# Optimization experiments

Measured on AMD Instinct MI355X. Metric: run time of the kernel, lower is better.

Reference implementation:

```python
import jax, jax.numpy as jnp
import numpy as np

N_NODES = 50000
N_EDGES = 800000
N_S = 32          # 0e channels in node feats
N_V = 16          # 1o channels in node feats
NB = 8            # radial bessel basis size
H = 64            # MLP hidden
S_OUT = N_S + N_V           # 48 scalar message channels (filtered 0e + dot path)
V_OUT = N_V + N_S + N_V     # 64 vector message channels (filtered 1o + sxY1 + vxY2)
NUM_IRREPS = S_OUT + V_OUT  # 112, gated by radial MLP
AVG_NEIGH = 16.0


def setup_inputs() -> dict:
    key = jax.random.key(0)
    ks = jax.random.split(key, 8)
    # scale so edge lengths fall mostly inside the envelope cutoff x_max=1
    vectors = jax.random.normal(ks[0], (N_EDGES, 3), jnp.float32) * 0.25
    node_s = jax.random.normal(ks[1], (N_NODES, N_S), jnp.float32)
    node_v = jax.random.normal(ks[2], (N_NODES, N_V, 3), jnp.float32)
    senders = jax.random.randint(ks[3], (N_EDGES,), 0, N_NODES)
    receivers = jax.random.randint(ks[4], (N_EDGES,), 0, N_NODES)
    W0 = jax.random.normal(ks[5], (NB, H), jnp.float32)
    W1 = jax.random.normal(ks[6], (H, H), jnp.float32)
    W2 = jax.random.normal(ks[7], (H, NUM_IRREPS), jnp.float32)
    return {"vectors": vectors, "node_s": node_s, "node_v": node_v,
            "W0": W0, "W1": W1, "W2": W2,
            "senders": senders, "receivers": receivers}


def _radial_embed(r):
    # r: [E,1] edge lengths. Bessel basis (x_max=1) * polynomial envelope, 0 at r==0.
    n = jnp.arange(1, NB + 1, dtype=r.dtype)            # [NB]
    safe_r = jnp.maximum(r, 1e-12)
    basis = jnp.sqrt(2.0) * jnp.sin(jnp.pi * n * r) / safe_r   # [E,NB]
    x = r
    env = (1.0 - 28.0 * x**6 + 48.0 * x**7 - 21.0 * x**8) * (x < 1.0)  # smooth cutoff
    return jnp.where(r == 0.0, 0.0, basis * env)        # [E,NB]


def reference(vectors, node_s, node_v, W0, W1, W2, senders, receivers):
    E = vectors.shape[0]
    r = jnp.linalg.norm(vectors, axis=-1, keepdims=True)          # [E,1]
    u = vectors / jnp.maximum(r, 1e-12)                            # unit vectors [E,3]

    # gather sender features
    s = node_s[senders]                                            # [E,N_S]
    v = node_v[senders]                                            # [E,N_V,3]

    # equivariant tensor-product paths against spherical harmonics of u
    # (filtered to target irreps 0e,1o). Y1 ~ u, Y2 ~ traceless u u^T.
    path_a = s[:, :, None] * u[:, None, :]                         # 0e x Y1 -> 1o [E,N_S,3]
    path_b = jnp.einsum('eci,ei->ec', v, u)                        # 1o x Y1 -> 0e [E,N_V]
    T = u[:, :, None] * u[:, None, :] - jnp.eye(3, dtype=u.dtype) / 3.0  # [E,3,3]
    path_c = jnp.sqrt(1.5) * jnp.einsum('eij,ecj->eci', T, v)      # 1o x Y2 -> 1o [E,N_V,3]

    msg_s = jnp.concatenate([s, path_b], axis=-1)                  # [E,S_OUT]
    msg_v = jnp.concatenate([v, path_a, path_c], axis=1)           # [E,V_OUT,3]

    # radial MLP gate (no bias, fan-in scaled, swish hidden, linear output)
    emb = _radial_embed(r)                                         # [E,NB]
    h = jax.nn.swish(emb @ W0 / jnp.sqrt(jnp.asarray(NB, emb.dtype)))
    h = jax.nn.swish(h @ W1 / jnp.sqrt(jnp.asarray(H, emb.dtype)))
    mix = h @ W2 / jnp.sqrt(jnp.asarray(H, emb.dtype))             # [E,NUM_IRREPS]

    msg_s = msg_s * mix[:, :S_OUT]
    msg_v = msg_v * mix[:, S_OUT:, None]

    # scatter-add to receivers
    n = node_s.shape[0]
    out_s = jnp.zeros((n, S_OUT), msg_s.dtype).at[receivers].add(msg_s)
    out_v = jnp.zeros((n, V_OUT, 3), msg_v.dtype).at[receivers].add(msg_v)

    inv = 1.0 / jnp.sqrt(AVG_NEIGH)
    return jnp.concatenate([out_s * inv, (out_v * inv).reshape(n, V_OUT * 3)], axis=-1)
```

## Files before the change

### kernel.cpp

```cpp
#include <hip/hip_runtime.h>
#include <hip/hip_fp16.h>

#define N_S 32
#define N_V 16
#define NB 8
#define HH 64
#define NIR 112
#define ROW 240
#define MROW 120
#define GCAP 64

typedef _Float16 half8 __attribute__((ext_vector_type(8)));
typedef _Float16 half4v __attribute__((ext_vector_type(4)));
typedef float f32x4 __attribute__((ext_vector_type(4)));

#define H8F(arr, idx) ((float)arr[(idx) >> 3][(idx) & 7])

__device__ __forceinline__ float swishf(float x) {
  return x / (1.f + __expf(-x));
}

struct ChanDesc { int path, off, mixI, i; };

__device__ __forceinline__ void mkDesc(int t, ChanDesc& d) {
  if (t < 32) { d.path = 0; d.off = t; d.mixI = t; d.i = 0; }
  else if (t < 48) { d.path = 1; d.off = 3 * (t - 32); d.mixI = t; d.i = 0; }
  else if (t < ROW) {
    int q = t - 48, c = q / 3, i = q - 3 * c;
    d.mixI = 48 + c;
    if (c < 16) { d.path = 2; d.off = q; d.i = 0; }
    else if (c < 48) { d.path = 3; d.off = c - 16; d.i = i; }
    else { d.path = 4; d.off = 3 * (c - 48); d.i = i; }
  } else { d.path = -1; d.off = 0; d.mixI = 0; d.i = 0; }
}

__device__ __forceinline__ float evalChan(const ChanDesc& d,
                                          const float* __restrict__ srow,
                                          const float* __restrict__ vrow,
                                          float mix, float u0, float u1, float u2) {
  if (d.path < 0) return 0.f;
  if (d.path == 0) return srow[d.off] * mix;
  if (d.path == 2) return vrow[d.off] * mix;
  float uo = d.i == 0 ? u0 : (d.i == 1 ? u1 : u2);
  if (d.path == 3) return srow[d.off] * uo * mix;
  float dd = vrow[d.off] * u0 + vrow[d.off + 1] * u1 + vrow[d.off + 2] * u2;
  if (d.path == 1) return dd * mix;
  return 1.22474487139f * (uo * dd - vrow[d.off + d.i] * 0.33333333333f) * mix;
}

__device__ __forceinline__ float evalChan16(const ChanDesc& d,
                                            const _Float16* __restrict__ srow,
                                            const _Float16* __restrict__ vrow,
                                            float mix, float u0, float u1, float u2) {
  if (d.path == 0) return (float)srow[d.off] * mix;
  if (d.path == 2) return (float)vrow[d.off] * mix;
  float uo = d.i == 0 ? u0 : (d.i == 1 ? u1 : u2);
  if (d.path == 3) return (float)srow[d.off] * uo * mix;
  float dd = (float)vrow[d.off] * u0 + (float)vrow[d.off + 1] * u1 + (float)vrow[d.off + 2] * u2;
  if (d.path == 1) return dd * mix;
  return 1.22474487139f * (uo * dd - (float)vrow[d.off + d.i] * 0.33333333333f) * mix;
}

__device__ __forceinline__ void radialEmb(float x, float y, float z, bool valid,
                                          float* emb, float* u0, float* u1, float* u2) {
  float r2 = x * x + y * y + z * z;
  float r = sqrtf(r2);
  float invr = 1.f / fmaxf(r, 1e-12f);
  *u0 = x * invr; *u1 = y * invr; *u2 = z * invr;
  float env = 0.f;
  if (r < 1.f) {
    float r3 = r * r2;
    float r6 = r3 * r3;
    env = 1.f + r6 * (-28.f + (48.f - 21.f * r) * r);
  }
  float coef = 1.41421356237f * invr * env;
  if (!valid || r == 0.f) coef = 0.f;
  float ph = 3.14159265358979323846f * r;
  float s1 = __sinf(ph), c1 = __cosf(ph);
  float twc = 2.f * c1;
  float sp = 0.f, sc = s1;
#pragma unroll
  for (int n = 0; n < NB; ++n) {
    emb[n] = coef * sc;
    float sn = twc * sc - sp;
    sp = sc;
    sc = sn;
  }
}


__global__ __launch_bounds__(256) void hist_kernel(const int* __restrict__ rcv,
                                                   int* __restrict__ hist, int E) {
  int e = blockIdx.x * 256 + threadIdx.x;
  if (e < E) atomicAdd(&hist[rcv[e]], 1);
}

__global__ __launch_bounds__(256) void scan1_kernel(const int* __restrict__ hist,
                                                    int* __restrict__ scanTmp,
                                                    int* __restrict__ bsum, int N) {
  __shared__ int sh[256];
  int t = threadIdx.x;
  int i = blockIdx.x * 256 + t;
  sh[t] = (i < N) ? hist[i] : 0;
  __syncthreads();
#pragma unroll
  for (int off = 1; off < 256; off <<= 1) {
    int x = (t >= off) ? sh[t - off] : 0;
    __syncthreads();
    sh[t] += x;
    __syncthreads();
  }
  if (i < N) scanTmp[i] = sh[t];
  if (t == 255) bsum[blockIdx.x] = sh[255];
}

__global__ __launch_bounds__(256) void scan2_kernel(int* __restrict__ bsum, int nb) {
  __shared__ int sh[256];
  int t = threadIdx.x;
  sh[t] = (t < nb) ? bsum[t] : 0;
  __syncthreads();
#pragma unroll
  for (int off = 1; off < 256; off <<= 1) {
    int x = (t >= off) ? sh[t - off] : 0;
    __syncthreads();
    sh[t] += x;
    __syncthreads();
  }
  int excl = (t == 0) ? 0 : sh[t - 1];
  if (t < nb) bsum[t] = excl;
}

__global__ __launch_bounds__(256) void scan3_kernel(const int* __restrict__ scanTmp,
                                                    const int* __restrict__ bsum,
                                                    const int* __restrict__ hist,
                                                    int* __restrict__ offs,
                                                    int* __restrict__ cursor, int N) {
  int i = blockIdx.x * 256 + threadIdx.x;
  if (i < N) {
    int incl = scanTmp[i] + bsum[blockIdx.x];
    offs[i + 1] = incl;
    cursor[i] = incl - hist[i];
    if (i == 0) offs[0] = 0;
  }
}

__global__ __launch_bounds__(256) void reorderInv_kernel(const int* __restrict__ rcv,
                                                         int* __restrict__ cursor,
                                                         int* __restrict__ invPos, int E) {
  int e = blockIdx.x * 256 + threadIdx.x;
  if (e < E) {
    int pos = atomicAdd(&cursor[rcv[e]], 1);
    invPos[e] = pos;
  }
}


__global__ __launch_bounds__(256) void prep_kernel(const float* __restrict__ W1,
                                                   const float* __restrict__ W2,
                                                   const float* __restrict__ ns,
                                                   const float* __restrict__ nv,
                                                   _Float16* __restrict__ W1T,
                                                   _Float16* __restrict__ W2T,
                                                   _Float16* __restrict__ s16,
                                                   _Float16* __restrict__ v16, int N) {
  int i = blockIdx.x * 256 + threadIdx.x;
  int ts = N * N_S;
  int tv = N * N_V * 3;
  if (i < ts) s16[i] = (_Float16)ns[i];
  else if (i < ts + tv) v16[i - ts] = (_Float16)nv[i - ts];
  else if (i < ts + tv + 4096) {
    int j = i - ts - tv;
    int k = j >> 6, n = j & 63;
    W1T[n * 64 + k] = (_Float16)(W1[k * 64 + n] * 0.125f);
  } else if (i < ts + tv + 4096 + 7168) {
    int j = i - ts - tv - 4096;
    int k = j / 112, n = j - k * 112;
    W2T[n * 64 + k] = (_Float16)(W2[k * 112 + n] * 0.125f);
  }
}

__global__ __launch_bounds__(256, 2) void mlp_msg_kernel(
    const float* __restrict__ vec,
    const float* __restrict__ W0,
    const _Float16* __restrict__ W1T,
    const _Float16* __restrict__ W2T,
    const int* __restrict__ senders,
    const int* __restrict__ invPos,
    const _Float16* __restrict__ s16,
    const _Float16* __restrict__ v16,
    _Float16* __restrict__ msgS,
    int E) {
  __shared__ __align__(16) _Float16 hbuf[4 * 64 * 72];
  const int lane = threadIdx.x & 63;
  const int wave = threadIdx.x >> 6;
  const int gbase = blockIdx.x * 256 + wave * 64;
  _Float16* hb = hbuf + wave * (64 * 72);

  const int m15 = lane & 15;
  const int q = lane >> 4;

  int e = gbase + lane;
  bool valid = e < E;
  float x = 0.f, y = 0.f, z = 0.f;
  int snd = 0, pos = 0;
  if (valid) {
    const float* vp = vec + 3 * (size_t)e;
    x = vp[0]; y = vp[1]; z = vp[2];
    snd = senders[e];
    pos = invPos[e];
  }
  float emb[NB], u0, u1, u2;
  radialEmb(x, y, z, valid, emb, &u0, &u1, &u2);

  for (int kg = 0; kg < 8; ++kg) {
    half8 pk;
#pragma unroll
    for (int kk = 0; kk < 8; ++kk) {
      int k = kg * 8 + kk;
      float a = 0.f;
#pragma unroll
      for (int n = 0; n < NB; ++n) a = fmaf(emb[n], W0[n * HH + k], a);
      pk[kk] = (_Float16)swishf(a * 0.35355339059f);
    }
    *(half8*)(hb + lane * 72 + kg * 8) = pk;
  }

  half8 ss[4], vv[6];
  {
    const _Float16* sp = s16 + (size_t)snd * N_S;
    const _Float16* vp16 = v16 + (size_t)snd * (N_V * 3);
#pragma unroll
    for (int k = 0; k < 4; ++k) ss[k] = *(const half8*)(sp + k * 8);
#pragma unroll
    for (int k = 0; k < 6; ++k) vv[k] = *(const half8*)(vp16 + k * 8);
  }

  {
    half8 bW1[4][2];
#pragma unroll
    for (int nt = 0; nt < 4; ++nt)
#pragma unroll
      for (int q2 = 0; q2 < 2; ++q2)
        bW1[nt][q2] = *(const half8*)(W1T + (nt * 16 + m15) * 64 + q2 * 32 + q * 8);
#pragma unroll
    for (int t = 0; t < 4; ++t) {
      half8 a0 = *(const half8*)(hb + (t * 16 + m15) * 72 + q * 8);
      half8 a1 = *(const half8*)(hb + (t * 16 + m15) * 72 + 32 + q * 8);
#pragma unroll
      for (int nt = 0; nt < 4; ++nt) {
        f32x4 d = {0.f, 0.f, 0.f, 0.f};
        d = __builtin_amdgcn_mfma_f32_16x16x32_f16(a0, bW1[nt][0], d, 0, 0, 0);
        d = __builtin_amdgcn_mfma_f32_16x16x32_f16(a1, bW1[nt][1], d, 0, 0, 0);
#pragma unroll
        for (int r = 0; r < 4; ++r)
          hb[(t * 16 + q * 4 + r) * 72 + nt * 16 + m15] = (_Float16)swishf(d[r]);
      }
    }
  }

  half8 A2[4][2];
#pragma unroll
  for (int t = 0; t < 4; ++t)
#pragma unroll
    for (int q2 = 0; q2 < 2; ++q2)
      A2[t][q2] = *(const half8*)(hb + (t * 16 + m15) * 72 + q2 * 32 + q * 8);

  float d16[16];
#pragma unroll
  for (int j = 0; j < 16; ++j)
    d16[j] = H8F(vv, 3 * j) * u0 + H8F(vv, 3 * j + 1) * u1 + H8F(vv, 3 * j + 2) * u2;

  _Float16* orow = msgS + (size_t)pos * ROW;

  for (int nl = 0; nl < 4; ++nl) {
    half8 b0 = *(const half8*)(W2T + (nl * 16 + m15) * 64 + q * 8);
    half8 b1 = *(const half8*)(W2T + (nl * 16 + m15) * 64 + 32 + q * 8);
#pragma unroll
    for (int t = 0; t < 4; ++t) {
      f32x4 d = {0.f, 0.f, 0.f, 0.f};
      d = __builtin_amdgcn_mfma_f32_16x16x32_f16(A2[t][0], b0, d, 0, 0, 0);
      d = __builtin_amdgcn_mfma_f32_16x16x32_f16(A2[t][1], b1, d, 0, 0, 0);
#pragma unroll
      for (int r = 0; r < 4; ++r)
        hb[(t * 16 + q * 4 + r) * 72 + nl * 16 + m15] = (_Float16)d[r];
    }
  }
  half8 m0[8];
#pragma unroll
  for (int k = 0; k < 8; ++k) m0[k] = *(const half8*)(hb + lane * 72 + k * 8);

  for (int nl = 0; nl < 3; ++nl) {
    int ntg = 4 + nl;
    half8 b0 = *(const half8*)(W2T + (ntg * 16 + m15) * 64 + q * 8);
    half8 b1 = *(const half8*)(W2T + (ntg * 16 + m15) * 64 + 32 + q * 8);
#pragma unroll
    for (int t = 0; t < 4; ++t) {
      f32x4 d = {0.f, 0.f, 0.f, 0.f};
      d = __builtin_amdgcn_mfma_f32_16x16x32_f16(A2[t][0], b0, d, 0, 0, 0);
      d = __builtin_amdgcn_mfma_f32_16x16x32_f16(A2[t][1], b1, d, 0, 0, 0);
#pragma unroll
      for (int r = 0; r < 4; ++r)
        hb[(t * 16 + q * 4 + r) * 72 + nl * 16 + m15] = (_Float16)d[r];
    }
  }

#pragma unroll
  for (int ck = 0; ck < 12; ++ck) {
    half8 outv;
#pragma unroll
    for (int jj = 0; jj < 8; ++jj) {
      const int t = ck * 8 + jj;
      float val;
      if (t < 32) {
        val = H8F(m0, t) * H8F(ss, t);
      } else if (t < 48) {
        val = H8F(m0, t) * d16[t - 32];
      } else {
        const int c = (t - 48) / 3;
        val = H8F(m0, 48 + c) * H8F(vv, t - 48);
      }
      outv[jj] = (_Float16)val;
    }
    if (valid) *(half8*)(orow + ck * 8) = outv;
  }

  half8 m1[6];
#pragma unroll
  for (int k = 0; k < 6; ++k) m1[k] = *(const half8*)(hb + lane * 72 + k * 8);
#pragma unroll
  for (int ck = 0; ck < 18; ++ck) {
    half8 outv;
#pragma unroll
    for (int jj = 0; jj < 8; ++jj) {
      const int t = 96 + ck * 8 + jj;
      const int c = (t - 48) / 3;
      const int i = (t - 48) % 3;
      const float uo = (i == 0) ? u0 : ((i == 1) ? u1 : u2);
      const float m = H8F(m1, c - 16);
      float val;
      if (c < 48) {
        val = m * H8F(ss, c - 16) * uo;
      } else {
        val = 1.22474487139f * (uo * d16[c - 48] - H8F(vv, t - 192) * 0.33333333333f) * m;
      }
      outv[jj] = (_Float16)val;
    }
    if (valid) *(half8*)(orow + 96 + ck * 8) = outv;
  }
}


__global__ __launch_bounds__(256) void gather_stream_kernel(
    const _Float16* __restrict__ msgS,
    const int* __restrict__ offs,
    float* __restrict__ out, int N) {
  int wid = blockIdx.x * 4 + (threadIdx.x >> 6);
  int lane = threadIdx.x & 63;
  if (wid >= N) return;
  int s0 = __builtin_amdgcn_readfirstlane(offs[wid]);
  int s1 = __builtin_amdgcn_readfirstlane(offs[wid + 1]);
  const bool act = lane < 60;

  float a0 = 0.f, a1 = 0.f, a2 = 0.f, a3 = 0.f;
  const _Float16* base = msgS + (size_t)s0 * ROW + lane * 4;
  const int n = s1 - s0;
  int j = 0;
  for (; j + 2 <= n; j += 2) {
    half4v va = {0, 0, 0, 0}, vb = {0, 0, 0, 0};
    if (act) {
      va = *(const half4v*)(base + (size_t)j * ROW);
      vb = *(const half4v*)(base + (size_t)(j + 1) * ROW);
    }
    a0 += (float)va[0] + (float)vb[0];
    a1 += (float)va[1] + (float)vb[1];
    a2 += (float)va[2] + (float)vb[2];
    a3 += (float)va[3] + (float)vb[3];
  }
  if (j < n && act) {
    half4v va = *(const half4v*)(base + (size_t)j * ROW);
    a0 += (float)va[0]; a1 += (float)va[1]; a2 += (float)va[2]; a3 += (float)va[3];
  }
  if (act) {
    float4 o = make_float4(0.25f * a0, 0.25f * a1, 0.25f * a2, 0.25f * a3);
    *(float4*)(out + (size_t)wid * ROW + lane * 4) = o;
  }
}


__global__ __launch_bounds__(256, 4) void mlp_mfma_sorted_kernel(
    const float* __restrict__ vec,
    const float* __restrict__ W0,
    const _Float16* __restrict__ W1T,
    const _Float16* __restrict__ W2T,
    const int* __restrict__ senders,
    const int* __restrict__ invPos,
    _Float16* __restrict__ mixS,
    int E) {
  __shared__ __align__(16) _Float16 hbuf[4 * 64 * 72];
  const int lane = threadIdx.x & 63;
  const int wave = threadIdx.x >> 6;
  const int gbase = blockIdx.x * 256 + wave * 64;
  _Float16* hb = hbuf + wave * (64 * 72);

  const int m15 = lane & 15;
  const int q = lane >> 4;

  {
    int e = gbase + lane;
    bool valid = e < E;
    float x = 0.f, y = 0.f, z = 0.f;
    int snd = 0;
    if (valid) {
      const float* vp = vec + 3 * (size_t)e;
      x = vp[0]; y = vp[1]; z = vp[2];
      snd = senders[e];
    }
    float emb[NB], u0, u1, u2;
    radialEmb(x, y, z, valid, emb, &u0, &u1, &u2);
    for (int kg = 0; kg < 8; ++kg) {
      half8 pk;
#pragma unroll
      for (int kk = 0; kk < 8; ++kk) {
        int k = kg * 8 + kk;
        float a = 0.f;
#pragma unroll
        for (int n = 0; n < NB; ++n) a = fmaf(emb[n], W0[n * HH + k], a);
        pk[kk] = (_Float16)swishf(a * 0.35355339059f);
      }
      *(half8*)(hb + lane * 72 + kg * 8) = pk;
    }
    float* auxp = (float*)(hb + lane * 72 + 64);
    auxp[0] = u0; auxp[1] = u1; auxp[2] = u2;
    ((int*)auxp)[3] = snd;
  }

  half8 bW1[4][2];
#pragma unroll
  for (int nt = 0; nt < 4; ++nt)
#pragma unroll
    for (int q2 = 0; q2 < 2; ++q2)
      bW1[nt][q2] = *(const half8*)(W1T + (nt * 16 + m15) * 64 + q2 * 32 + q * 8);

#pragma unroll
  for (int t = 0; t < 4; ++t) {
    half8 a0 = *(const half8*)(hb + (t * 16 + m15) * 72 + q * 8);
    half8 a1 = *(const half8*)(hb + (t * 16 + m15) * 72 + 32 + q * 8);
#pragma unroll
    for (int nt = 0; nt < 4; ++nt) {
      f32x4 d = {0.f, 0.f, 0.f, 0.f};
      d = __builtin_amdgcn_mfma_f32_16x16x32_f16(a0, bW1[nt][0], d, 0, 0, 0);
      d = __builtin_amdgcn_mfma_f32_16x16x32_f16(a1, bW1[nt][1], d, 0, 0, 0);
#pragma unroll
      for (int r = 0; r < 4; ++r)
        hb[(t * 16 + q * 4 + r) * 72 + nt * 16 + m15] = (_Float16)swishf(d[r]);
    }
  }

  half8 A2[4][2];
#pragma unroll
  for (int t = 0; t < 4; ++t)
#pragma unroll
    for (int q2 = 0; q2 < 2; ++q2)
      A2[t][q2] = *(const half8*)(hb + (t * 16 + m15) * 72 + q2 * 32 + q * 8);

  for (int nl = 0; nl < 4; ++nl) {
    half8 b0 = *(const half8*)(W2T + (nl * 16 + m15) * 64 + q * 8);
    half8 b1 = *(const half8*)(W2T + (nl * 16 + m15) * 64 + 32 + q * 8);
#pragma unroll
    for (int t = 0; t < 4; ++t) {
      f32x4 d = {0.f, 0.f, 0.f, 0.f};
      d = __builtin_amdgcn_mfma_f32_16x16x32_f16(A2[t][0], b0, d, 0, 0, 0);
      d = __builtin_amdgcn_mfma_f32_16x16x32_f16(A2[t][1], b1, d, 0, 0, 0);
#pragma unroll
      for (int r = 0; r < 4; ++r)
        hb[(t * 16 + q * 4 + r) * 72 + nl * 16 + m15] = (_Float16)d[r];
    }
  }
  for (int it = 0; it < 8; ++it) {
    int c = it * 64 + lane;
    int el = c >> 3, p = c & 7;
    int e = gbase + el;
    half8 v = *(const half8*)(hb + el * 72 + p * 8);
    if (e < E) {
      int pos = invPos[e];
      *(half8*)(mixS + (size_t)pos * MROW + p * 8) = v;
    }
  }

  for (int nl = 0; nl < 3; ++nl) {
    int ntg = 4 + nl;
    half8 b0 = *(const half8*)(W2T + (ntg * 16 + m15) * 64 + q * 8);
    half8 b1 = *(const half8*)(W2T + (ntg * 16 + m15) * 64 + 32 + q * 8);
#pragma unroll
    for (int t = 0; t < 4; ++t) {
      f32x4 d = {0.f, 0.f, 0.f, 0.f};
      d = __builtin_amdgcn_mfma_f32_16x16x32_f16(A2[t][0], b0, d, 0, 0, 0);
      d = __builtin_amdgcn_mfma_f32_16x16x32_f16(A2[t][1], b1, d, 0, 0, 0);
#pragma unroll
      for (int r = 0; r < 4; ++r)
        hb[(t * 16 + q * 4 + r) * 72 + nl * 16 + m15] = (_Float16)d[r];
    }
  }
  for (int it = 0; it < 7; ++it) {
    int c = it * 64 + lane;
    int el = (int)(((unsigned)c * 9363u) >> 16);
    int p = c - el * 7;
    int e = gbase + el;
    half8 v = *(const half8*)(hb + el * 72 + (p < 6 ? p * 8 : 64));
    if (e < E) {
      int pos = invPos[e];
      *(half8*)(mixS + (size_t)pos * MROW + 64 + p * 8) = v;
    }
  }
}

__global__ __launch_bounds__(256) void gather_lds_kernel(
    const _Float16* __restrict__ mixS,
    const _Float16* __restrict__ s16,
    const _Float16* __restrict__ v16,
    const int* __restrict__ offs,
    float* __restrict__ out, int N) {
  __shared__ __align__(16) _Float16 mixLds[GCAP * MROW];
  __shared__ __align__(16) _Float16 nodeLds[GCAP * 80];

  const int tid = threadIdx.x;
  const int lane = tid & 63;
  const int wave = tid >> 6;
  const int wid0 = blockIdx.x * 4;

  const int e0 = offs[wid0];
  const int e4 = offs[min(wid0 + 4, N)];
  const int wid = wid0 + wave;
  const int sw = offs[min(wid, N)];
  const int ew = offs[min(wid + 1, N)];

  ChanDesc d[4];
#pragma unroll
  for (int tb = 0; tb < 4; ++tb) mkDesc(tb * 64 + lane, d[tb]);

  float acc[4] = {0.f, 0.f, 0.f, 0.f};

  for (int c0 = e0; c0 < e4; c0 += GCAP) {
    const int cnt = min(GCAP, e4 - c0);
    for (int ch = tid; ch < cnt * 15; ch += 256) {
      int row = ch / 15, part = ch - row * 15;
      *(half8*)(mixLds + row * MROW + part * 8) =
          *(const half8*)(mixS + (size_t)(c0 + row) * MROW + part * 8);
    }
    __syncthreads();
    for (int ch = tid; ch < cnt * 10; ch += 256) {
      int row = ch / 10, part = ch - row * 10;
      int snd = ((const int*)(mixLds + row * MROW + 112))[3];
      const _Float16* src = (part < 4)
          ? s16 + (size_t)snd * N_S + part * 8
          : v16 + (size_t)snd * (N_V * 3) + (part - 4) * 8;
      *(half8*)(nodeLds + row * 80 + (part < 4 ? part * 8 : 32 + (part - 4) * 8)) =
          *(const half8*)src;
    }
    __syncthreads();
    const int jlo = max(sw - c0, 0);
    const int jhi = min(ew - c0, cnt);
    for (int j = jlo; j < jhi; ++j) {
      const _Float16* row = mixLds + j * MROW;
      const float* aux = (const float*)(row + 112);
      float u0 = aux[0], u1 = aux[1], u2 = aux[2];
      const _Float16* srow = nodeLds + j * 80;
      const _Float16* vrow = srow + 32;
#pragma unroll
      for (int tb = 0; tb < 4; ++tb) {
        if (d[tb].path >= 0) {
          float m = (float)row[d[tb].mixI];
          acc[tb] += evalChan16(d[tb], srow, vrow, m, u0, u1, u2);
        }
      }
    }
    __syncthreads();
  }

  if (wid < N) {
    float* orow = out + (size_t)wid * ROW;
#pragma unroll
    for (int tb = 0; tb < 4; ++tb) {
      int t = tb * 64 + lane;
      if (t < ROW) orow[t] = 0.25f * acc[tb];
    }
  }
}


__global__ __launch_bounds__(64) void edge_kernel(
    const float* __restrict__ vec,
    const float* __restrict__ nodes_s,
    const float* __restrict__ nodes_v,
    const int* __restrict__ senders,
    const int* __restrict__ receivers,
    const float* __restrict__ W0f,
    const float* __restrict__ W1f,
    const float* __restrict__ W2f,
    float* __restrict__ out, int E) {
  __shared__ float hLds[HH * 64];
  __shared__ float uLds[64 * 3];
  __shared__ int sLds[64];
  __shared__ int rLds[64];
  __half* mixLds = reinterpret_cast<__half*>(hLds);

  const int lane = threadIdx.x;
  const int base = blockIdx.x * 64;
  const int eg = base + lane;
  const bool valid = eg < E;

  float emb[NB];
  {
    float x = 0.f, y = 0.f, z = 0.f;
    int snd = 0, rcv = 0;
    if (valid) {
      const float* vp = vec + 3 * (size_t)eg;
      x = vp[0]; y = vp[1]; z = vp[2];
      snd = senders[eg];
      rcv = receivers[eg];
    }
    float u0, u1, u2;
    radialEmb(x, y, z, valid, emb, &u0, &u1, &u2);
    uLds[lane * 3 + 0] = u0;
    uLds[lane * 3 + 1] = u1;
    uLds[lane * 3 + 2] = u2;
    sLds[lane] = snd;
    rLds[lane] = rcv;
  }

  for (int j0 = 0; j0 < HH; j0 += 8) {
    float a[8];
#pragma unroll
    for (int jj = 0; jj < 8; ++jj) a[jj] = 0.f;
#pragma unroll
    for (int k = 0; k < NB; ++k) {
      const float* wrow = W0f + k * HH + j0;
      float ek = emb[k];
#pragma unroll
      for (int jj = 0; jj < 8; ++jj) a[jj] = fmaf(ek, wrow[jj], a[jj]);
    }
#pragma unroll
    for (int jj = 0; jj < 8; ++jj)
      hLds[(j0 + jj) * 64 + lane] = swishf(a[jj] * 0.35355339059f);
  }
  __syncthreads();

  float h2[HH];
#pragma unroll
  for (int j = 0; j < HH; ++j) h2[j] = 0.f;
  for (int k = 0; k < HH; ++k) {
    float hk = hLds[k * 64 + lane];
    const float* wrow = W1f + k * HH;
#pragma unroll
    for (int j = 0; j < HH; ++j) h2[j] = fmaf(hk, wrow[j], h2[j]);
  }
#pragma unroll
  for (int j = 0; j < HH; ++j) h2[j] = swishf(h2[j] * 0.125f);
  __syncthreads();

  for (int m0 = 0; m0 < NIR; m0 += 4) {
    float a0 = 0.f, a1 = 0.f, a2 = 0.f, a3 = 0.f;
#pragma unroll
    for (int k = 0; k < HH; ++k) {
      const float* wrow = W2f + k * NIR + m0;
      float hk = h2[k];
      a0 = fmaf(hk, wrow[0], a0);
      a1 = fmaf(hk, wrow[1], a1);
      a2 = fmaf(hk, wrow[2], a2);
      a3 = fmaf(hk, wrow[3], a3);
    }
    mixLds[lane * NIR + m0 + 0] = __float2half_rn(a0 * 0.125f);
    mixLds[lane * NIR + m0 + 1] = __float2half_rn(a1 * 0.125f);
    mixLds[lane * NIR + m0 + 2] = __float2half_rn(a2 * 0.125f);
    mixLds[lane * NIR + m0 + 3] = __float2half_rn(a3 * 0.125f);
  }
  __syncthreads();

  ChanDesc d[4];
#pragma unroll
  for (int tb = 0; tb < 4; ++tb) mkDesc(tb * 64 + lane, d[tb]);

  const int cnt = min(64, E - base);
  for (int e = 0; e < cnt; ++e) {
    int snd = sLds[e], rcv = rLds[e];
    float u0 = uLds[e * 3 + 0], u1 = uLds[e * 3 + 1], u2 = uLds[e * 3 + 2];
    const float* srow = nodes_s + (size_t)snd * N_S;
    const float* vrow = nodes_v + (size_t)snd * (N_V * 3);
    const __half* mrow = mixLds + e * NIR;
    float* orow = out + (size_t)rcv * ROW;
#pragma unroll
    for (int tb = 0; tb < 4; ++tb) {
      if (d[tb].path >= 0) {
        float m = __half2float(mrow[d[tb].mixI]);
        float val = evalChan(d[tb], srow, vrow, m, u0, u1, u2);
        unsafeAtomicAdd(orow + tb * 64 + lane, 0.25f * val);
      }
    }
  }
}


extern "C" void kernel_launch(void* const* d_in, const int* in_sizes, int n_in,
                              void* d_out, int out_size, void* d_ws, size_t ws_size,
                              hipStream_t stream) {
  const float* vec = (const float*)d_in[0];
  const float* ns = (const float*)d_in[1];
  const float* nv = (const float*)d_in[2];
  const float* w0 = (const float*)d_in[3];
  const float* w1 = (const float*)d_in[4];
  const float* w2 = (const float*)d_in[5];
  const int* snd = (const int*)d_in[6];
  const int* rcv = (const int*)d_in[7];
  float* out = (float*)d_out;

  const int E = in_sizes[6];
  const int N = in_sizes[1] / N_S;
  const int nb = (N + 255) / 256;
  const int eb = (E + 255) / 256;
  const int prepElems = N * (N_S + N_V * 3) + 4096 + 7168;

  {
    char* p = (char*)d_ws;
    _Float16* msgS = (_Float16*)p;  p += (size_t)E * ROW * sizeof(_Float16);
    int* hist = (int*)p;            p += (size_t)N * 4;
    int* scanTmp = (int*)p;         p += (size_t)N * 4;
    int* offs = (int*)p;            p += ((size_t)N + 1) * 4;
    int* cursor = (int*)p;          p += (size_t)N * 4;
    int* bsum = (int*)p;            p += 256 * 4;
    int* invPos = (int*)p;          p += (size_t)E * 4;
    p = (char*)(((uintptr_t)p + 15) & ~(uintptr_t)15);
    _Float16* W1T = (_Float16*)p;   p += 4096 * sizeof(_Float16);
    _Float16* W2T = (_Float16*)p;   p += 7168 * sizeof(_Float16);
    _Float16* s16 = (_Float16*)p;   p += (size_t)N * N_S * sizeof(_Float16);
    _Float16* v16 = (_Float16*)p;   p += (size_t)N * N_V * 3 * sizeof(_Float16);
    size_t needA = (size_t)(p - (char*)d_ws);

    if (needA <= ws_size && nb <= 256) {
      hipMemsetAsync(hist, 0, (size_t)N * 4, stream);
      hist_kernel<<<eb, 256, 0, stream>>>(rcv, hist, E);
      scan1_kernel<<<nb, 256, 0, stream>>>(hist, scanTmp, bsum, N);
      scan2_kernel<<<1, 256, 0, stream>>>(bsum, nb);
      scan3_kernel<<<nb, 256, 0, stream>>>(scanTmp, bsum, hist, offs, cursor, N);
      reorderInv_kernel<<<eb, 256, 0, stream>>>(rcv, cursor, invPos, E);
      prep_kernel<<<(prepElems + 255) / 256, 256, 0, stream>>>(w1, w2, ns, nv, W1T, W2T, s16, v16, N);
      mlp_msg_kernel<<<eb, 256, 0, stream>>>(vec, w0, W1T, W2T, snd, invPos, s16, v16, msgS, E);
      gather_stream_kernel<<<(N + 3) / 4, 256, 0, stream>>>(msgS, offs, out, N);
      return;
    }
  }

  {
    char* p = (char*)d_ws;
    _Float16* mixS = (_Float16*)p;  p += (size_t)E * MROW * sizeof(_Float16);
    int* hist = (int*)p;            p += (size_t)N * 4;
    int* scanTmp = (int*)p;         p += (size_t)N * 4;
    int* offs = (int*)p;            p += ((size_t)N + 1) * 4;
    int* cursor = (int*)p;          p += (size_t)N * 4;
    int* bsum = (int*)p;            p += 256 * 4;
    int* invPos = (int*)p;          p += (size_t)E * 4;
    p = (char*)(((uintptr_t)p + 15) & ~(uintptr_t)15);
    _Float16* W1T = (_Float16*)p;   p += 4096 * sizeof(_Float16);
    _Float16* W2T = (_Float16*)p;   p += 7168 * sizeof(_Float16);
    _Float16* s16 = (_Float16*)p;   p += (size_t)N * N_S * sizeof(_Float16);
    _Float16* v16 = (_Float16*)p;   p += (size_t)N * N_V * 3 * sizeof(_Float16);
    size_t needB = (size_t)(p - (char*)d_ws);

    if (needB <= ws_size && nb <= 256) {
      hipMemsetAsync(hist, 0, (size_t)N * 4, stream);
      hist_kernel<<<eb, 256, 0, stream>>>(rcv, hist, E);
      scan1_kernel<<<nb, 256, 0, stream>>>(hist, scanTmp, bsum, N);
      scan2_kernel<<<1, 256, 0, stream>>>(bsum, nb);
      scan3_kernel<<<nb, 256, 0, stream>>>(scanTmp, bsum, hist, offs, cursor, N);
      reorderInv_kernel<<<eb, 256, 0, stream>>>(rcv, cursor, invPos, E);
      prep_kernel<<<(prepElems + 255) / 256, 256, 0, stream>>>(w1, w2, ns, nv, W1T, W2T, s16, v16, N);
      mlp_mfma_sorted_kernel<<<eb, 256, 0, stream>>>(vec, w0, W1T, W2T, snd, invPos, mixS, E);
      gather_lds_kernel<<<(N + 3) / 4, 256, 0, stream>>>(mixS, s16, v16, offs, out, N);
      return;
    }
  }

  hipMemsetAsync(d_out, 0, (size_t)out_size * sizeof(float), stream);
  edge_kernel<<<(E + 63) / 64, 64, 0, stream>>>(vec, ns, nv, snd, rcv, w0, w1, w2, out, E);
}
```

Before: 557.9 us.

## Chunk edge messages into fp32 passes processed in sorted receiver order

Replaces the inverse-position scatter with a sorted order array, so the message kernel reads edges in receiver order and writes rows contiguously. Messages are now staged in fp32, and the edge set is split into up to 16 passes so each staging buffer fits the workspace. Each pass is followed by a gather kernel that accumulates partial sums into the output. This trades fp16 staging for higher precision and a smaller, possibly cache-resident buffer. It adds read-modify-write traffic on the output across passes, a full gather launch per pass, and scattered per-edge reads of vectors and senders.

```diff
diff --git a/kernel.cpp b/kernel.cpp
--- a/kernel.cpp
+++ b/kernel.cpp
@@ -151,6 +151,16 @@
   if (e < E) {
     int pos = atomicAdd(&cursor[rcv[e]], 1);
     invPos[e] = pos;
+  }
+}
+
+__global__ __launch_bounds__(256) void reorderOrd_kernel(const int* __restrict__ rcv,
+                                                         int* __restrict__ cursor,
+                                                         int* __restrict__ order, int E) {
+  int e = blockIdx.x * 256 + threadIdx.x;
+  if (e < E) {
+    int pos = atomicAdd(&cursor[rcv[e]], 1);
+    order[pos] = e;
   }
 }
 
@@ -179,17 +189,17 @@
   }
 }
 
-__global__ __launch_bounds__(256, 2) void mlp_msg_kernel(
+__global__ __launch_bounds__(256, 2) void mlp_msg_pass_kernel(
     const float* __restrict__ vec,
     const float* __restrict__ W0,
     const _Float16* __restrict__ W1T,
     const _Float16* __restrict__ W2T,
     const int* __restrict__ senders,
-    const int* __restrict__ invPos,
+    const int* __restrict__ order,
     const _Float16* __restrict__ s16,
     const _Float16* __restrict__ v16,
-    _Float16* __restrict__ msgS,
-    int E) {
+    float* __restrict__ msgS,
+    int P0, int P1) {
   __shared__ __align__(16) _Float16 hbuf[4 * 64 * 72];
   const int lane = threadIdx.x & 63;
   const int wave = threadIdx.x >> 6;
@@ -199,15 +209,15 @@
   const int m15 = lane & 15;
   const int q = lane >> 4;
 
-  int e = gbase + lane;
-  bool valid = e < E;
+  const int pos = P0 + gbase + lane;
+  const bool valid = pos < P1;
   float x = 0.f, y = 0.f, z = 0.f;
-  int snd = 0, pos = 0;
+  int snd = 0;
   if (valid) {
+    int e = order[pos];
     const float* vp = vec + 3 * (size_t)e;
     x = vp[0]; y = vp[1]; z = vp[2];
     snd = senders[e];
-    pos = invPos[e];
   }
   float emb[NB], u0, u1, u2;
   radialEmb(x, y, z, valid, emb, &u0, &u1, &u2);
@@ -270,7 +280,7 @@
   for (int j = 0; j < 16; ++j)
     d16[j] = H8F(vv, 3 * j) * u0 + H8F(vv, 3 * j + 1) * u1 + H8F(vv, 3 * j + 2) * u2;
 
-  _Float16* orow = msgS + (size_t)pos * ROW;
+  float* orow = msgS + (size_t)(gbase + lane) * ROW;
 
   for (int nl = 0; nl < 4; ++nl) {
     half8 b0 = *(const half8*)(W2T + (nl * 16 + m15) * 64 + q * 8);
@@ -306,7 +316,7 @@
 
 #pragma unroll
   for (int ck = 0; ck < 12; ++ck) {
-    half8 outv;
+    f32x4 o0, o1;
 #pragma unroll
     for (int jj = 0; jj < 8; ++jj) {
       const int t = ck * 8 + jj;
@@ -319,9 +329,12 @@
         const int c = (t - 48) / 3;
         val = H8F(m0, 48 + c) * H8F(vv, t - 48);
       }
-      outv[jj] = (_Float16)val;
-    }
-    if (valid) *(half8*)(orow + ck * 8) = outv;
+      if (jj < 4) o0[jj] = val; else o1[jj - 4] = val;
+    }
+    if (valid) {
+      *(f32x4*)(orow + ck * 8) = o0;
+      *(f32x4*)(orow + ck * 8 + 4) = o1;
+    }
   }
 
   half8 m1[6];
@@ -329,7 +342,7 @@
   for (int k = 0; k < 6; ++k) m1[k] = *(const half8*)(hb + lane * 72 + k * 8);
 #pragma unroll
   for (int ck = 0; ck < 18; ++ck) {
-    half8 outv;
+    f32x4 o0, o1;
 #pragma unroll
     for (int jj = 0; jj < 8; ++jj) {
       const int t = 96 + ck * 8 + jj;
@@ -343,46 +356,52 @@
       } else {
         val = 1.22474487139f * (uo * d16[c - 48] - H8F(vv, t - 192) * 0.33333333333f) * m;
       }
-      outv[jj] = (_Float16)val;
-    }
-    if (valid) *(half8*)(orow + 96 + ck * 8) = outv;
-  }
-}
-
+      if (jj < 4) o0[jj] = val; else o1[jj - 4] = val;
+    }
+    if (valid) {
+      *(f32x4*)(orow + 96 + ck * 8) = o0;
+      *(f32x4*)(orow + 96 + ck * 8 + 4) = o1;
+    }
+  }
+}
 
 __global__ __launch_bounds__(256) void gather_stream_kernel(
-    const _Float16* __restrict__ msgS,
+    const float* __restrict__ msgS,
     const int* __restrict__ offs,
-    float* __restrict__ out, int N) {
+    float* __restrict__ out, int N, int P0, int P1, int isFirst) {
   int wid = blockIdx.x * 4 + (threadIdx.x >> 6);
   int lane = threadIdx.x & 63;
   if (wid >= N) return;
   int s0 = __builtin_amdgcn_readfirstlane(offs[wid]);
   int s1 = __builtin_amdgcn_readfirstlane(offs[wid + 1]);
+  const int lo = max(s0, P0);
+  const int hi = min(s1, P1);
+  const bool ownZero = (s0 == s1) && isFirst;
+  if (lo >= hi && !ownZero) return;
+  const bool first = s0 >= P0;
   const bool act = lane < 60;
 
-  float a0 = 0.f, a1 = 0.f, a2 = 0.f, a3 = 0.f;
-  const _Float16* base = msgS + (size_t)s0 * ROW + lane * 4;
-  const int n = s1 - s0;
+  f32x4 acc = {0.f, 0.f, 0.f, 0.f};
+  const float* base = msgS + (size_t)(lo - P0) * ROW + lane * 4;
+  const int n = hi - lo;
   int j = 0;
   for (; j + 2 <= n; j += 2) {
-    half4v va = {0, 0, 0, 0}, vb = {0, 0, 0, 0};
+    f32x4 va = {0.f, 0.f, 0.f, 0.f}, vb = {0.f, 0.f, 0.f, 0.f};
     if (act) {
-      va = *(const half4v*)(base + (size_t)j * ROW);
-      vb = *(const half4v*)(base + (size_t)(j + 1) * ROW);
-    }
-    a0 += (float)va[0] + (float)vb[0];
-    a1 += (float)va[1] + (float)vb[1];
-    a2 += (float)va[2] + (float)vb[2];
-    a3 += (float)va[3] + (float)vb[3];
+      va = *(const f32x4*)(base + (size_t)j * ROW);
+      vb = *(const f32x4*)(base + (size_t)(j + 1) * ROW);
+    }
+    acc += va + vb;
   }
   if (j < n && act) {
-    half4v va = *(const half4v*)(base + (size_t)j * ROW);
-    a0 += (float)va[0]; a1 += (float)va[1]; a2 += (float)va[2]; a3 += (float)va[3];
+    acc += *(const f32x4*)(base + (size_t)j * ROW);
   }
   if (act) {
-    float4 o = make_float4(0.25f * a0, 0.25f * a1, 0.25f * a2, 0.25f * a3);
-    *(float4*)(out + (size_t)wid * ROW + lane * 4) = o;
+    float* op = out + (size_t)wid * ROW + lane * 4;
+    f32x4 o = {0.f, 0.f, 0.f, 0.f};
+    if (!first) o = *(const f32x4*)op;
+    o += 0.25f * acc;
+    *(f32x4*)op = o;
   }
 }
 
@@ -719,34 +738,43 @@
   const int eb = (E + 255) / 256;
   const int prepElems = N * (N_S + N_V * 3) + 4096 + 7168;
 
-  {
+  for (int P = 1; P <= 16; ++P) {
+    const size_t chunk = ((size_t)E + P - 1) / (size_t)P;
     char* p = (char*)d_ws;
-    _Float16* msgS = (_Float16*)p;  p += (size_t)E * ROW * sizeof(_Float16);
+    float* msgS = (float*)p;        p += chunk * ROW * sizeof(float);
     int* hist = (int*)p;            p += (size_t)N * 4;
     int* scanTmp = (int*)p;         p += (size_t)N * 4;
     int* offs = (int*)p;            p += ((size_t)N + 1) * 4;
     int* cursor = (int*)p;          p += (size_t)N * 4;
     int* bsum = (int*)p;            p += 256 * 4;
-    int* invPos = (int*)p;          p += (size_t)E * 4;
+    int* order = (int*)p;           p += (size_t)E * 4;
     p = (char*)(((uintptr_t)p + 15) & ~(uintptr_t)15);
     _Float16* W1T = (_Float16*)p;   p += 4096 * sizeof(_Float16);
     _Float16* W2T = (_Float16*)p;   p += 7168 * sizeof(_Float16);
     _Float16* s16 = (_Float16*)p;   p += (size_t)N * N_S * sizeof(_Float16);
     _Float16* v16 = (_Float16*)p;   p += (size_t)N * N_V * 3 * sizeof(_Float16);
-    size_t needA = (size_t)(p - (char*)d_ws);
-
-    if (needA <= ws_size && nb <= 256) {
-      hipMemsetAsync(hist, 0, (size_t)N * 4, stream);
-      hist_kernel<<<eb, 256, 0, stream>>>(rcv, hist, E);
-      scan1_kernel<<<nb, 256, 0, stream>>>(hist, scanTmp, bsum, N);
-      scan2_kernel<<<1, 256, 0, stream>>>(bsum, nb);
-      scan3_kernel<<<nb, 256, 0, stream>>>(scanTmp, bsum, hist, offs, cursor, N);
-      reorderInv_kernel<<<eb, 256, 0, stream>>>(rcv, cursor, invPos, E);
-      prep_kernel<<<(prepElems + 255) / 256, 256, 0, stream>>>(w1, w2, ns, nv, W1T, W2T, s16, v16, N);
-      mlp_msg_kernel<<<eb, 256, 0, stream>>>(vec, w0, W1T, W2T, snd, invPos, s16, v16, msgS, E);
-      gather_stream_kernel<<<(N + 3) / 4, 256, 0, stream>>>(msgS, offs, out, N);
-      return;
-    }
+    size_t need = (size_t)(p - (char*)d_ws);
+    if (need > ws_size || nb > 256) continue;
+
+    hipMemsetAsync(hist, 0, (size_t)N * 4, stream);
+    hist_kernel<<<eb, 256, 0, stream>>>(rcv, hist, E);
+    scan1_kernel<<<nb, 256, 0, stream>>>(hist, scanTmp, bsum, N);
+    scan2_kernel<<<1, 256, 0, stream>>>(bsum, nb);
+    scan3_kernel<<<nb, 256, 0, stream>>>(scanTmp, bsum, hist, offs, cursor, N);
+    reorderOrd_kernel<<<eb, 256, 0, stream>>>(rcv, cursor, order, E);
+    prep_kernel<<<(prepElems + 255) / 256, 256, 0, stream>>>(w1, w2, ns, nv, W1T, W2T, s16, v16, N);
+
+    for (int k = 0; k < P; ++k) {
+      const int P0 = (int)((size_t)k * chunk);
+      if (P0 >= E) break;
+      const int P1 = (int)min((size_t)E, (size_t)P0 + chunk);
+      const int cnt = P1 - P0;
+      mlp_msg_pass_kernel<<<(cnt + 255) / 256, 256, 0, stream>>>(
+          vec, w0, W1T, W2T, snd, order, s16, v16, msgS, P0, P1);
+      gather_stream_kernel<<<(N + 3) / 4, 256, 0, stream>>>(
+          msgS, offs, out, N, P0, P1, k == 0 ? 1 : 0);
+    }
+    return;
   }
 
   {
```

Result: slower. 676.8 us (+21.3%).
